# Kernel optimization log

Measured on AMD Instinct MI355X. Metric: run time of the kernel, lower is better.

Reference implementation:

```python
import jax, jax.numpy as jnp
import numpy as np

S, B, C = 7, 2, 20
LAMBDA_COORD = 5.0
LAMBDA_NOOBJ = 0.5
EPS = 1e-6


def _to_abs_xyxy(boxes):
    # boxes: [..., S, S, 4] cell-relative (x,y,w,h) -> normalized image (x1,y1,x2,y2)
    col = jnp.arange(S, dtype=boxes.dtype)            # broadcasts over last grid axis
    row = jnp.arange(S, dtype=boxes.dtype)[:, None]   # broadcasts over second-to-last grid axis
    x, y, w, h = boxes[..., 0], boxes[..., 1], boxes[..., 2], boxes[..., 3]
    cx = (col + x) / S
    cy = (row + y) / S
    return jnp.stack([cx - w / 2, cy - h / 2, cx + w / 2, cy + h / 2], axis=-1)


def _iou(a, b):
    # elementwise IoU of corresponding xyxy boxes (broadcasting allowed)
    x1 = jnp.maximum(a[..., 0], b[..., 0])
    y1 = jnp.maximum(a[..., 1], b[..., 1])
    x2 = jnp.minimum(a[..., 2], b[..., 2])
    y2 = jnp.minimum(a[..., 3], b[..., 3])
    inter = jnp.clip(x2 - x1, 0.0) * jnp.clip(y2 - y1, 0.0)
    area_a = (a[..., 2] - a[..., 0]) * (a[..., 3] - a[..., 1])
    area_b = (b[..., 2] - b[..., 0]) * (b[..., 3] - b[..., 1])
    return inter / (area_a + area_b - inter + EPS)


def setup_inputs() -> dict:
    key = jax.random.key(0)
    kp, kb, kf, kc = jax.random.split(key, 4)
    bs = 16384
    predictions = jax.random.uniform(kp, (bs, S, S, B * 5 + C), dtype=jnp.float32)
    gt_box = jax.random.uniform(kb, (bs, S, S, 4), dtype=jnp.float32)
    obj = (jax.random.uniform(kf, (bs, S, S)) < 0.06).astype(jnp.float32)
    cls = jax.nn.one_hot(jax.random.randint(kc, (bs, S, S), 0, C), C, dtype=jnp.float32)
    targets = jnp.concatenate([gt_box, obj[..., None], cls], axis=-1)
    return {"predictions": predictions, "targets": targets}


def reference(predictions, targets):
    bs = predictions.shape[0]
    pb = predictions[..., : B * 5].reshape(bs, S, S, B, 5)
    boxes = pb[..., :4]                 # [bs,S,S,B,4]
    confs = pb[..., 4]                  # [bs,S,S,B]
    logits = predictions[..., B * 5 :]  # [bs,S,S,C]

    gt_boxes = targets[..., :4]
    objf = (targets[..., 4] > 0).astype(predictions.dtype)  # [bs,S,S]
    gt_cls = targets[..., 5:]

    # IoU per candidate box vs the cell's GT box
    gt_abs = _to_abs_xyxy(gt_boxes)                         # [bs,S,S,4]
    pred_abs = _to_abs_xyxy(jnp.moveaxis(boxes, 3, 1))      # [bs,B,S,S,4]
    ious = jnp.moveaxis(_iou(pred_abs, gt_abs[:, None]), 1, 3)  # [bs,S,S,B]

    best = jnp.argmax(ious, axis=-1)                        # [bs,S,S]
    resp_box = jnp.take_along_axis(boxes, best[..., None, None], axis=3)[..., 0, :]  # [bs,S,S,4]
    resp_conf = jnp.take_along_axis(confs, best[..., None], axis=-1)[..., 0]
    resp_iou = jnp.take_along_axis(ious, best[..., None], axis=-1)[..., 0]

    # Localization loss (masked-sum == torch boolean-mask + sum reduction)
    w = objf[..., None]
    xy_loss = jnp.sum(w * (resp_box[..., :2] - gt_boxes[..., :2]) ** 2)
    wh_loss = jnp.sum(w * (jnp.sqrt(resp_box[..., 2:4] + EPS) - jnp.sqrt(gt_boxes[..., 2:4] + EPS)) ** 2)
    loss_coord = xy_loss + wh_loss

    # Objectness confidence: target is (detached) IoU of responsible box
    loss_conf_obj = jnp.sum(objf * (resp_conf - jax.lax.stop_gradient(resp_iou)) ** 2)

    # No-object confidence: every (cell, box) that is not the responsible box of an object cell
    resp_mask = jax.nn.one_hot(best, B, dtype=predictions.dtype) * objf[..., None]  # [bs,S,S,B]
    loss_conf_noobj = jnp.sum((1.0 - resp_mask) * confs ** 2)

    # Classification: cross-entropy with one-hot GT, summed over object cells
    logp = jax.nn.log_softmax(logits, axis=-1)
    loss_class = -jnp.sum(objf * jnp.sum(gt_cls * logp, axis=-1))

    n = jnp.asarray(bs, predictions.dtype)
    loss_total = (LAMBDA_COORD * loss_coord + loss_conf_obj + LAMBDA_NOOBJ * loss_conf_noobj + loss_class) / n
    # [loss_coord, loss_conf_obj, loss_conf_noobj, loss_class, loss_total]
    return jnp.stack([loss_coord / n, loss_conf_obj / n, loss_conf_noobj / n, loss_class / n, loss_total])
```

## Files before the change

### kernel.cpp

```cpp
#include <hip/hip_runtime.h>
#include <math.h>

namespace {
constexpr int S = 7;
constexpr int B = 2;
constexpr int C = 20;
constexpr int PF = B * 5 + C;
constexpr int TF = 5 + C;
constexpr float EPS = 1e-6f;
constexpr float LAMBDA_COORD = 5.0f;
constexpr float LAMBDA_NOOBJ = 0.5f;
constexpr int BLK = 256;
}

__global__ __launch_bounds__(BLK) void k_main(const float* __restrict__ pred,
                                              const float* __restrict__ tgt,
                                              float* __restrict__ part,
                                              int n_cells) {
    const int tid = threadIdx.x;
    const int cell = blockIdx.x * BLK + tid;

    float v0 = 0.f, v1 = 0.f, v2 = 0.f, v3 = 0.f;
    if (cell < n_cells) {
        const float* p = pred + (size_t)cell * PF;
        const float* t = tgt + (size_t)cell * TF;

        const float2 p45 = *(const float2*)(p + 4);
        const float2 p89 = *(const float2*)(p + 8);
        const float c0 = p45.x, c1 = p89.y;
        const float t4 = t[4];

        v2 = c0 * c0 + c1 * c1;

        if (t4 > 0.f) {
            const int j = cell % S;
            const int i = (cell / S) % S;
            const float invS = 1.0f / (float)S;

            const float2 p01 = *(const float2*)(p + 0);
            const float2 p23 = *(const float2*)(p + 2);
            const float2 p67 = *(const float2*)(p + 6);
            const float gx = t[0], gy = t[1], gw = t[2], gh = t[3];

            const float gcx = ((float)j + gx) * invS;
            const float gcy = ((float)i + gy) * invS;
            const float gx1 = gcx - gw * 0.5f, gy1 = gcy - gh * 0.5f;
            const float gx2 = gcx + gw * 0.5f, gy2 = gcy + gh * 0.5f;
            const float garea = (gx2 - gx1) * (gy2 - gy1);

            const float bx[B]  = {p01.x, p45.y};
            const float by[B]  = {p01.y, p67.x};
            const float bw_[B] = {p23.x, p67.y};
            const float bh[B]  = {p23.y, p89.x};
            const float cf[B]  = {c0, c1};
            float iou[B];
            #pragma unroll
            for (int b = 0; b < B; ++b) {
                const float cx = ((float)j + bx[b]) * invS;
                const float cy = ((float)i + by[b]) * invS;
                const float x1 = cx - bw_[b] * 0.5f, y1 = cy - bh[b] * 0.5f;
                const float x2 = cx + bw_[b] * 0.5f, y2 = cy + bh[b] * 0.5f;
                const float ix1 = fmaxf(x1, gx1), iy1 = fmaxf(y1, gy1);
                const float ix2 = fminf(x2, gx2), iy2 = fminf(y2, gy2);
                const float inter = fmaxf(ix2 - ix1, 0.f) * fmaxf(iy2 - iy1, 0.f);
                const float parea = (x2 - x1) * (y2 - y1);
                iou[b] = inter / (parea + garea - inter + EPS);
            }
            const int best = (iou[1] > iou[0]) ? 1 : 0;
            const float rconf = cf[best], riou = iou[best];

            const float dx = bx[best] - gx, dy = by[best] - gy;
            const float swd = sqrtf(bw_[best] + EPS) - sqrtf(gw + EPS);
            const float shd = sqrtf(bh[best] + EPS) - sqrtf(gh + EPS);
            v0 = dx*dx + dy*dy + swd*swd + shd*shd;
            const float dc = rconf - riou;
            v1 = dc * dc;
            v2 -= rconf * rconf;

            float se = 0.f, dot = 0.f, sg = 0.f;
            #pragma unroll
            for (int c = 0; c < C; c += 2) {
                const float2 lc = *(const float2*)(p + 10 + c);
                const float g0 = t[5 + c], g1 = t[6 + c];
                se  += __expf(lc.x) + __expf(lc.y);
                dot += g0 * lc.x + g1 * lc.y;
                sg  += g0 + g1;
            }
            v3 = __logf(se) * sg - dot;
        }
    }

    float v[4] = {v0, v1, v2, v3};
    #pragma unroll
    for (int off = 32; off >= 1; off >>= 1) {
        v[0] += __shfl_down(v[0], off, 64);
        v[1] += __shfl_down(v[1], off, 64);
        v[2] += __shfl_down(v[2], off, 64);
        v[3] += __shfl_down(v[3], off, 64);
    }
    __shared__ float red[16];
    const int lane = tid & 63;
    const int wave = tid >> 6;
    if (lane == 0) {
        red[wave * 4 + 0] = v[0];
        red[wave * 4 + 1] = v[1];
        red[wave * 4 + 2] = v[2];
        red[wave * 4 + 3] = v[3];
    }
    __syncthreads();
    if (tid < 4)
        part[blockIdx.x * 4 + tid] =
            red[tid] + red[4 + tid] + red[8 + tid] + red[12 + tid];
}

__global__ __launch_bounds__(BLK) void k_fin(const float* __restrict__ part,
                                             float* __restrict__ out,
                                             int nblk, float n) {
    const int tid = threadIdx.x;
    float a0 = 0.f, a1 = 0.f, a2 = 0.f, a3 = 0.f;
    for (int r = tid; r < nblk; r += BLK) {
        const float4 q = *(const float4*)(part + r * 4);
        a0 += q.x; a1 += q.y; a2 += q.z; a3 += q.w;
    }
    float v[4] = {a0, a1, a2, a3};
    #pragma unroll
    for (int off = 32; off >= 1; off >>= 1) {
        v[0] += __shfl_down(v[0], off, 64);
        v[1] += __shfl_down(v[1], off, 64);
        v[2] += __shfl_down(v[2], off, 64);
        v[3] += __shfl_down(v[3], off, 64);
    }
    __shared__ float red[16];
    const int lane = tid & 63;
    const int wave = tid >> 6;
    if (lane == 0) {
        red[wave * 4 + 0] = v[0];
        red[wave * 4 + 1] = v[1];
        red[wave * 4 + 2] = v[2];
        red[wave * 4 + 3] = v[3];
    }
    __syncthreads();
    if (tid == 0) {
        const float coord  = red[0] + red[4] + red[8] + red[12];
        const float cobj   = red[1] + red[5] + red[9] + red[13];
        const float cnoobj = red[2] + red[6] + red[10] + red[14];
        const float ccls   = red[3] + red[7] + red[11] + red[15];
        const float inv = 1.0f / n;
        out[0] = coord * inv;
        out[1] = cobj * inv;
        out[2] = cnoobj * inv;
        out[3] = ccls * inv;
        out[4] = (LAMBDA_COORD * coord + cobj + LAMBDA_NOOBJ * cnoobj + ccls) * inv;
    }
}

extern "C" void kernel_launch(void* const* d_in, const int* in_sizes, int n_in,
                              void* d_out, int out_size, void* d_ws, size_t ws_size,
                              hipStream_t stream) {
    const float* pred = (const float*)d_in[0];
    const float* tgt  = (const float*)d_in[1];
    float* out  = (float*)d_out;
    float* part = (float*)d_ws;

    const int n_cells = in_sizes[0] / PF;
    const float bs = (float)(n_cells / (S * S));
    const int nblk = (n_cells + BLK - 1) / BLK;

    k_main<<<nblk, BLK, 0, stream>>>(pred, tgt, part, n_cells);
    k_fin<<<1, BLK, 0, stream>>>(part, out, nblk, bs);
}
```

Measured before the change: 201.5 us.

## Stream both inputs as coalesced float4 in a grid-stride scan

Replaces the one-thread-per-cell kernel with a fixed-size grid-stride kernel that reads the prediction and target arrays as flat coalesced float4 streams, with several loads in flight per thread. Confidence and objectness values are picked out by their position in each vector. Object cells then re-gather their full prediction and target rows for the IoU and class terms. The goal is fully coalesced bandwidth instead of strided per-cell loads. The cost is extra modulo arithmetic per vector, divergent branches, and a second read of the rows for object cells. Every byte of both arrays is now read, including box and logit fields that no-object cells never needed.

```diff
diff --git a/kernel.cpp b/kernel.cpp
--- a/kernel.cpp
+++ b/kernel.cpp
@@ -3,90 +3,122 @@
 
 namespace {
 constexpr int S = 7;
-constexpr int B = 2;
+constexpr int PF = 30;
+constexpr int TF = 25;
 constexpr int C = 20;
-constexpr int PF = B * 5 + C;
-constexpr int TF = 5 + C;
 constexpr float EPS = 1e-6f;
 constexpr float LAMBDA_COORD = 5.0f;
 constexpr float LAMBDA_NOOBJ = 0.5f;
 constexpr int BLK = 256;
-}
-
-__global__ __launch_bounds__(BLK) void k_main(const float* __restrict__ pred,
+constexpr int ILP = 4;
+constexpr int NBLK = 2048;
+}
+
+__global__ __launch_bounds__(BLK) void k_scan(const float* __restrict__ pred,
                                               const float* __restrict__ tgt,
                                               float* __restrict__ part,
-                                              int n_cells) {
-    const int tid = threadIdx.x;
-    const int cell = blockIdx.x * BLK + tid;
+                                              unsigned np4p, unsigned np4t) {
+    const unsigned tid = threadIdx.x;
+    const unsigned total = np4p + np4t;
+    const unsigned tile = BLK * ILP;
 
     float v0 = 0.f, v1 = 0.f, v2 = 0.f, v3 = 0.f;
-    if (cell < n_cells) {
-        const float* p = pred + (size_t)cell * PF;
-        const float* t = tgt + (size_t)cell * TF;
-
-        const float2 p45 = *(const float2*)(p + 4);
-        const float2 p89 = *(const float2*)(p + 8);
-        const float c0 = p45.x, c1 = p89.y;
-        const float t4 = t[4];
-
-        v2 = c0 * c0 + c1 * c1;
-
-        if (t4 > 0.f) {
-            const int j = cell % S;
-            const int i = (cell / S) % S;
-            const float invS = 1.0f / (float)S;
-
-            const float2 p01 = *(const float2*)(p + 0);
-            const float2 p23 = *(const float2*)(p + 2);
-            const float2 p67 = *(const float2*)(p + 6);
-            const float gx = t[0], gy = t[1], gw = t[2], gh = t[3];
-
-            const float gcx = ((float)j + gx) * invS;
-            const float gcy = ((float)i + gy) * invS;
-            const float gx1 = gcx - gw * 0.5f, gy1 = gcy - gh * 0.5f;
-            const float gx2 = gcx + gw * 0.5f, gy2 = gcy + gh * 0.5f;
-            const float garea = (gx2 - gx1) * (gy2 - gy1);
-
-            const float bx[B]  = {p01.x, p45.y};
-            const float by[B]  = {p01.y, p67.x};
-            const float bw_[B] = {p23.x, p67.y};
-            const float bh[B]  = {p23.y, p89.x};
-            const float cf[B]  = {c0, c1};
-            float iou[B];
-            #pragma unroll
-            for (int b = 0; b < B; ++b) {
-                const float cx = ((float)j + bx[b]) * invS;
-                const float cy = ((float)i + by[b]) * invS;
-                const float x1 = cx - bw_[b] * 0.5f, y1 = cy - bh[b] * 0.5f;
-                const float x2 = cx + bw_[b] * 0.5f, y2 = cy + bh[b] * 0.5f;
-                const float ix1 = fmaxf(x1, gx1), iy1 = fmaxf(y1, gy1);
-                const float ix2 = fminf(x2, gx2), iy2 = fminf(y2, gy2);
-                const float inter = fmaxf(ix2 - ix1, 0.f) * fmaxf(iy2 - iy1, 0.f);
-                const float parea = (x2 - x1) * (y2 - y1);
-                iou[b] = inter / (parea + garea - inter + EPS);
+
+    for (unsigned start = blockIdx.x * tile; start < total; start += gridDim.x * tile) {
+        float4 val[ILP];
+        unsigned qv[ILP];
+        bool okv[ILP], ispv[ILP];
+        #pragma unroll
+        for (int k = 0; k < ILP; ++k) {
+            const unsigned idx = start + (unsigned)k * BLK + tid;
+            const bool ok = idx < total;
+            const bool isp = idx < np4p;
+            const unsigned q = isp ? idx : (idx - np4p);
+            okv[k] = ok; ispv[k] = isp; qv[k] = q;
+            const float4* src = isp ? (const float4*)pred : (const float4*)tgt;
+            val[k] = ok ? src[q] : make_float4(0.f, 0.f, 0.f, 0.f);
+        }
+        #pragma unroll
+        for (int k = 0; k < ILP; ++k) {
+            if (!okv[k]) continue;
+            const float4 v = val[k];
+            const unsigned q = qv[k];
+            if (ispv[k]) {
+                const unsigned r = q % 15u;
+                const float s = (r == 1u) ? v.x
+                              : (r == 2u) ? v.y
+                              : (r == 8u) ? v.z
+                              : (r == 9u) ? v.w : 0.f;
+                v2 += s * s;
+            } else {
+                const unsigned r = q % 25u;
+                const unsigned m = q / 25u;
+                float t4 = 0.f; unsigned cell = 0u;
+                if (r == 1u)       { t4 = v.x; cell = 4u * m; }
+                else if (r == 7u)  { t4 = v.y; cell = 4u * m + 1u; }
+                else if (r == 13u) { t4 = v.z; cell = 4u * m + 2u; }
+                else if (r == 19u) { t4 = v.w; cell = 4u * m + 3u; }
+                if (t4 > 0.f) {
+                    const float* p = pred + (size_t)cell * PF;
+                    const float* t = tgt + (size_t)cell * TF;
+                    const unsigned j = cell % 7u;
+                    const unsigned i = (cell / 7u) % 7u;
+                    const float invS = 1.0f / 7.0f;
+
+                    const float2 p01 = *(const float2*)(p + 0);
+                    const float2 p23 = *(const float2*)(p + 2);
+                    const float2 p45 = *(const float2*)(p + 4);
+                    const float2 p67 = *(const float2*)(p + 6);
+                    const float2 p89 = *(const float2*)(p + 8);
+                    const float gx = t[0], gy = t[1], gw = t[2], gh = t[3];
+
+                    const float gcx = ((float)j + gx) * invS;
+                    const float gcy = ((float)i + gy) * invS;
+                    const float gx1 = gcx - gw * 0.5f, gy1 = gcy - gh * 0.5f;
+                    const float gx2 = gcx + gw * 0.5f, gy2 = gcy + gh * 0.5f;
+                    const float garea = (gx2 - gx1) * (gy2 - gy1);
+
+                    const float bx[2]  = {p01.x, p45.y};
+                    const float by[2]  = {p01.y, p67.x};
+                    const float bw_[2] = {p23.x, p67.y};
+                    const float bh[2]  = {p23.y, p89.x};
+                    const float cf[2]  = {p45.x, p89.y};
+                    float iou[2];
+                    #pragma unroll
+                    for (int b = 0; b < 2; ++b) {
+                        const float cx = ((float)j + bx[b]) * invS;
+                        const float cy = ((float)i + by[b]) * invS;
+                        const float x1 = cx - bw_[b] * 0.5f, y1 = cy - bh[b] * 0.5f;
+                        const float x2 = cx + bw_[b] * 0.5f, y2 = cy + bh[b] * 0.5f;
+                        const float ix1 = fmaxf(x1, gx1), iy1 = fmaxf(y1, gy1);
+                        const float ix2 = fminf(x2, gx2), iy2 = fminf(y2, gy2);
+                        const float inter = fmaxf(ix2 - ix1, 0.f) * fmaxf(iy2 - iy1, 0.f);
+                        const float parea = (x2 - x1) * (y2 - y1);
+                        iou[b] = inter / (parea + garea - inter + EPS);
+                    }
+                    const int best = (iou[1] > iou[0]) ? 1 : 0;
+                    const float rconf = cf[best], riou = iou[best];
+
+                    const float dx = bx[best] - gx, dy = by[best] - gy;
+                    const float swd = sqrtf(bw_[best] + EPS) - sqrtf(gw + EPS);
+                    const float shd = sqrtf(bh[best] + EPS) - sqrtf(gh + EPS);
+                    v0 += dx*dx + dy*dy + swd*swd + shd*shd;
+                    const float dc = rconf - riou;
+                    v1 += dc * dc;
+                    v2 -= rconf * rconf;
+
+                    float se = 0.f, dot = 0.f, sg = 0.f;
+                    #pragma unroll
+                    for (int c = 0; c < C; c += 2) {
+                        const float2 lc = *(const float2*)(p + 10 + c);
+                        const float g0 = t[5 + c], g1 = t[6 + c];
+                        se  += __expf(lc.x) + __expf(lc.y);
+                        dot += g0 * lc.x + g1 * lc.y;
+                        sg  += g0 + g1;
+                    }
+                    v3 += __logf(se) * sg - dot;
+                }
             }
-            const int best = (iou[1] > iou[0]) ? 1 : 0;
-            const float rconf = cf[best], riou = iou[best];
-
-            const float dx = bx[best] - gx, dy = by[best] - gy;
-            const float swd = sqrtf(bw_[best] + EPS) - sqrtf(gw + EPS);
-            const float shd = sqrtf(bh[best] + EPS) - sqrtf(gh + EPS);
-            v0 = dx*dx + dy*dy + swd*swd + shd*shd;
-            const float dc = rconf - riou;
-            v1 = dc * dc;
-            v2 -= rconf * rconf;
-
-            float se = 0.f, dot = 0.f, sg = 0.f;
-            #pragma unroll
-            for (int c = 0; c < C; c += 2) {
-                const float2 lc = *(const float2*)(p + 10 + c);
-                const float g0 = t[5 + c], g1 = t[6 + c];
-                se  += __expf(lc.x) + __expf(lc.y);
-                dot += g0 * lc.x + g1 * lc.y;
-                sg  += g0 + g1;
-            }
-            v3 = __logf(se) * sg - dot;
         }
     }
 
@@ -162,10 +194,11 @@
     float* out  = (float*)d_out;
     float* part = (float*)d_ws;
 
+    const unsigned np4p = (unsigned)(in_sizes[0] / 4);
+    const unsigned np4t = (unsigned)(in_sizes[1] / 4);
     const int n_cells = in_sizes[0] / PF;
     const float bs = (float)(n_cells / (S * S));
-    const int nblk = (n_cells + BLK - 1) / BLK;
-
-    k_main<<<nblk, BLK, 0, stream>>>(pred, tgt, part, n_cells);
-    k_fin<<<1, BLK, 0, stream>>>(part, out, nblk, bs);
-}
+
+    k_scan<<<NBLK, BLK, 0, stream>>>(pred, tgt, part, np4p, np4t);
+    k_fin<<<1, BLK, 0, stream>>>(part, out, NBLK, bs);
+}
```

Result: slower. 218.1 us (+8.2%).

## Split loss into dense no-object scan plus compacted object-cell worklist pass

Applied to the files above, without the earlier changes.

The single per-cell kernel is replaced by a grid-stride scan that reads predictions as coalesced float4 and accumulates confidence squares through per-lane masks, since the 30-float row period fits 15 float4 vectors. The same scan compacts object cells into a worklist with a global atomic counter, and a second kernel processes only those sparse cells to compute IoU, coordinate and class terms. The aim is to remove the strided scalar loads and the divergent work across the dense majority of cells. In exchange it adds extra launches, an atomic per object cell, and a fallback path used when the workspace is too small.

```diff
diff --git a/kernel.cpp b/kernel.cpp
--- a/kernel.cpp
+++ b/kernel.cpp
@@ -3,59 +3,248 @@
 
 namespace {
 constexpr int S = 7;
-constexpr int B = 2;
+constexpr int PF = 30;
+constexpr int TF = 25;
 constexpr int C = 20;
-constexpr int PF = B * 5 + C;
-constexpr int TF = 5 + C;
 constexpr float EPS = 1e-6f;
 constexpr float LAMBDA_COORD = 5.0f;
 constexpr float LAMBDA_NOOBJ = 0.5f;
 constexpr int BLK = 256;
-}
-
-__global__ __launch_bounds__(BLK) void k_main(const float* __restrict__ pred,
+constexpr int ILP = 4;
+constexpr int NBLK = 1875;
+constexpr int NBLK2 = 256;
+
+constexpr int OFF_PART  = 0;
+constexpr int OFF_PART2 = NBLK * 4;
+constexpr int OFF_CNT   = OFF_PART2 + NBLK2 * 4;
+constexpr int OFF_WL    = OFF_CNT + 4;
+}
+
+__global__ void k_zero(int* cnt) {
+    if (threadIdx.x == 0) *cnt = 0;
+}
+
+__global__ __launch_bounds__(BLK) void k_scan(const float4* __restrict__ pred4,
                                               const float* __restrict__ tgt,
                                               float* __restrict__ part,
-                                              int n_cells) {
+                                              int* __restrict__ cnt,
+                                              int* __restrict__ wl,
+                                              unsigned np4p, unsigned n_cells) {
+    const unsigned tid = threadIdx.x;
+    const unsigned stride = (unsigned)NBLK * BLK * ILP;
+    const unsigned base0 = blockIdx.x * (unsigned)(BLK * ILP) + tid;
+
+    float v2 = 0.f;
+
+    float mx[ILP], my[ILP], mz[ILP], mw[ILP];
+    #pragma unroll
+    for (int k = 0; k < ILP; ++k) {
+        const unsigned r = (base0 + (unsigned)k * BLK) % 15u;
+        mx[k] = (r == 1u) ? 1.f : 0.f;
+        my[k] = (r == 2u) ? 1.f : 0.f;
+        mz[k] = (r == 8u) ? 1.f : 0.f;
+        mw[k] = (r == 9u) ? 1.f : 0.f;
+    }
+    for (unsigned s = base0; s < np4p; s += stride) {
+        #pragma unroll
+        for (int k = 0; k < ILP; ++k) {
+            const unsigned idx = s + (unsigned)k * BLK;
+            if (idx < np4p) {
+                const float4 v = pred4[idx];
+                v2 += (mx[k] * v.x) * v.x + (my[k] * v.y) * v.y
+                    + (mz[k] * v.z) * v.z + (mw[k] * v.w) * v.w;
+            }
+        }
+    }
+
+    const unsigned gstride = (unsigned)NBLK * BLK;
+    for (unsigned cell = blockIdx.x * (unsigned)BLK + tid; cell < n_cells; cell += gstride) {
+        const float t4 = tgt[cell * 25u + 4u];
+        if (t4 > 0.f) {
+            const int pos = atomicAdd(cnt, 1);
+            wl[pos] = (int)cell;
+        }
+    }
+
+    #pragma unroll
+    for (int off = 32; off >= 1; off >>= 1) v2 += __shfl_down(v2, off, 64);
+    __shared__ float red[4];
+    if ((tid & 63) == 0) red[tid >> 6] = v2;
+    __syncthreads();
+    if (tid < 4) {
+        const float s2 = red[0] + red[1] + red[2] + red[3];
+        part[blockIdx.x * 4 + tid] = (tid == 2) ? s2 : 0.f;
+    }
+}
+
+__global__ __launch_bounds__(BLK) void k_obj(const float* __restrict__ pred,
+                                             const float* __restrict__ tgt,
+                                             const int* __restrict__ cnt,
+                                             const int* __restrict__ wl,
+                                             float* __restrict__ part2) {
+    const int tid = threadIdx.x;
+    const int n = *cnt;
+    float v0 = 0.f, v1 = 0.f, v2 = 0.f, v3 = 0.f;
+
+    for (int w = blockIdx.x * BLK + tid; w < n; w += NBLK2 * BLK) {
+        const unsigned cell = (unsigned)wl[w];
+        const float* p = pred + (size_t)cell * PF;
+        const float* t = tgt + (size_t)cell * TF;
+        const unsigned j = cell % 7u;
+        const unsigned i = (cell / 7u) % 7u;
+        const float invS = 1.0f / 7.0f;
+
+        const float2 p01 = *(const float2*)(p + 0);
+        const float2 p23 = *(const float2*)(p + 2);
+        const float2 p45 = *(const float2*)(p + 4);
+        const float2 p67 = *(const float2*)(p + 6);
+        const float2 p89 = *(const float2*)(p + 8);
+        const float gx = t[0], gy = t[1], gw = t[2], gh = t[3];
+
+        const float gcx = ((float)j + gx) * invS;
+        const float gcy = ((float)i + gy) * invS;
+        const float gx1 = gcx - gw * 0.5f, gy1 = gcy - gh * 0.5f;
+        const float gx2 = gcx + gw * 0.5f, gy2 = gcy + gh * 0.5f;
+        const float garea = (gx2 - gx1) * (gy2 - gy1);
+
+        const float bx[2]  = {p01.x, p45.y};
+        const float by[2]  = {p01.y, p67.x};
+        const float bw_[2] = {p23.x, p67.y};
+        const float bh[2]  = {p23.y, p89.x};
+        const float cf[2]  = {p45.x, p89.y};
+        float iou[2];
+        #pragma unroll
+        for (int b = 0; b < 2; ++b) {
+            const float cx = ((float)j + bx[b]) * invS;
+            const float cy = ((float)i + by[b]) * invS;
+            const float x1 = cx - bw_[b] * 0.5f, y1 = cy - bh[b] * 0.5f;
+            const float x2 = cx + bw_[b] * 0.5f, y2 = cy + bh[b] * 0.5f;
+            const float ix1 = fmaxf(x1, gx1), iy1 = fmaxf(y1, gy1);
+            const float ix2 = fminf(x2, gx2), iy2 = fminf(y2, gy2);
+            const float inter = fmaxf(ix2 - ix1, 0.f) * fmaxf(iy2 - iy1, 0.f);
+            const float parea = (x2 - x1) * (y2 - y1);
+            iou[b] = inter / (parea + garea - inter + EPS);
+        }
+        const int best = (iou[1] > iou[0]) ? 1 : 0;
+        const float rconf = cf[best], riou = iou[best];
+
+        const float dx = bx[best] - gx, dy = by[best] - gy;
+        const float swd = sqrtf(bw_[best] + EPS) - sqrtf(gw + EPS);
+        const float shd = sqrtf(bh[best] + EPS) - sqrtf(gh + EPS);
+        v0 += dx * dx + dy * dy + swd * swd + shd * shd;
+        const float dc = rconf - riou;
+        v1 += dc * dc;
+        v2 -= rconf * rconf;
+
+        float se = 0.f, dot = 0.f, sg = 0.f;
+        #pragma unroll
+        for (int c = 0; c < C; c += 2) {
+            const float2 lc = *(const float2*)(p + 10 + c);
+            const float g0 = t[5 + c], g1 = t[6 + c];
+            se  += __expf(lc.x) + __expf(lc.y);
+            dot += g0 * lc.x + g1 * lc.y;
+            sg  += g0 + g1;
+        }
+        v3 += __logf(se) * sg - dot;
+    }
+
+    float v[4] = {v0, v1, v2, v3};
+    #pragma unroll
+    for (int off = 32; off >= 1; off >>= 1) {
+        v[0] += __shfl_down(v[0], off, 64);
+        v[1] += __shfl_down(v[1], off, 64);
+        v[2] += __shfl_down(v[2], off, 64);
+        v[3] += __shfl_down(v[3], off, 64);
+    }
+    __shared__ float red[16];
+    if ((tid & 63) == 0) {
+        const int wv = tid >> 6;
+        red[wv * 4 + 0] = v[0];
+        red[wv * 4 + 1] = v[1];
+        red[wv * 4 + 2] = v[2];
+        red[wv * 4 + 3] = v[3];
+    }
+    __syncthreads();
+    if (tid < 4)
+        part2[blockIdx.x * 4 + tid] =
+            red[tid] + red[4 + tid] + red[8 + tid] + red[12 + tid];
+}
+
+__global__ __launch_bounds__(BLK) void k_fin(const float* __restrict__ part,
+                                             float* __restrict__ out,
+                                             int nslots, float n) {
+    const int tid = threadIdx.x;
+    float a0 = 0.f, a1 = 0.f, a2 = 0.f, a3 = 0.f;
+    for (int r = tid; r < nslots; r += BLK) {
+        const float4 q = *(const float4*)(part + r * 4);
+        a0 += q.x; a1 += q.y; a2 += q.z; a3 += q.w;
+    }
+    float v[4] = {a0, a1, a2, a3};
+    #pragma unroll
+    for (int off = 32; off >= 1; off >>= 1) {
+        v[0] += __shfl_down(v[0], off, 64);
+        v[1] += __shfl_down(v[1], off, 64);
+        v[2] += __shfl_down(v[2], off, 64);
+        v[3] += __shfl_down(v[3], off, 64);
+    }
+    __shared__ float red[16];
+    if ((tid & 63) == 0) {
+        const int wv = tid >> 6;
+        red[wv * 4 + 0] = v[0];
+        red[wv * 4 + 1] = v[1];
+        red[wv * 4 + 2] = v[2];
+        red[wv * 4 + 3] = v[3];
+    }
+    __syncthreads();
+    if (tid == 0) {
+        const float coord  = red[0] + red[4] + red[8] + red[12];
+        const float cobj   = red[1] + red[5] + red[9] + red[13];
+        const float cnoobj = red[2] + red[6] + red[10] + red[14];
+        const float ccls   = red[3] + red[7] + red[11] + red[15];
+        const float inv = 1.0f / n;
+        out[0] = coord * inv;
+        out[1] = cobj * inv;
+        out[2] = cnoobj * inv;
+        out[3] = ccls * inv;
+        out[4] = (LAMBDA_COORD * coord + cobj + LAMBDA_NOOBJ * cnoobj + ccls) * inv;
+    }
+}
+
+__global__ __launch_bounds__(BLK) void k_main_fb(const float* __restrict__ pred,
+                                                 const float* __restrict__ tgt,
+                                                 float* __restrict__ part,
+                                                 int n_cells) {
     const int tid = threadIdx.x;
     const int cell = blockIdx.x * BLK + tid;
-
     float v0 = 0.f, v1 = 0.f, v2 = 0.f, v3 = 0.f;
     if (cell < n_cells) {
         const float* p = pred + (size_t)cell * PF;
         const float* t = tgt + (size_t)cell * TF;
-
         const float2 p45 = *(const float2*)(p + 4);
         const float2 p89 = *(const float2*)(p + 8);
         const float c0 = p45.x, c1 = p89.y;
-        const float t4 = t[4];
-
         v2 = c0 * c0 + c1 * c1;
-
-        if (t4 > 0.f) {
+        if (t[4] > 0.f) {
             const int j = cell % S;
             const int i = (cell / S) % S;
             const float invS = 1.0f / (float)S;
-
             const float2 p01 = *(const float2*)(p + 0);
             const float2 p23 = *(const float2*)(p + 2);
             const float2 p67 = *(const float2*)(p + 6);
             const float gx = t[0], gy = t[1], gw = t[2], gh = t[3];
-
             const float gcx = ((float)j + gx) * invS;
             const float gcy = ((float)i + gy) * invS;
             const float gx1 = gcx - gw * 0.5f, gy1 = gcy - gh * 0.5f;
             const float gx2 = gcx + gw * 0.5f, gy2 = gcy + gh * 0.5f;
             const float garea = (gx2 - gx1) * (gy2 - gy1);
-
-            const float bx[B]  = {p01.x, p45.y};
-            const float by[B]  = {p01.y, p67.x};
-            const float bw_[B] = {p23.x, p67.y};
-            const float bh[B]  = {p23.y, p89.x};
-            const float cf[B]  = {c0, c1};
-            float iou[B];
+            const float bx[2]  = {p01.x, p45.y};
+            const float by[2]  = {p01.y, p67.x};
+            const float bw_[2] = {p23.x, p67.y};
+            const float bh[2]  = {p23.y, p89.x};
+            const float cf[2]  = {c0, c1};
+            float iou[2];
             #pragma unroll
-            for (int b = 0; b < B; ++b) {
+            for (int b = 0; b < 2; ++b) {
                 const float cx = ((float)j + bx[b]) * invS;
                 const float cy = ((float)i + by[b]) * invS;
                 const float x1 = cx - bw_[b] * 0.5f, y1 = cy - bh[b] * 0.5f;
@@ -68,7 +257,6 @@
             }
             const int best = (iou[1] > iou[0]) ? 1 : 0;
             const float rconf = cf[best], riou = iou[best];
-
             const float dx = bx[best] - gx, dy = by[best] - gy;
             const float swd = sqrtf(bw_[best] + EPS) - sqrtf(gw + EPS);
             const float shd = sqrtf(bh[best] + EPS) - sqrtf(gh + EPS);
@@ -76,7 +264,6 @@
             const float dc = rconf - riou;
             v1 = dc * dc;
             v2 -= rconf * rconf;
-
             float se = 0.f, dot = 0.f, sg = 0.f;
             #pragma unroll
             for (int c = 0; c < C; c += 2) {
@@ -89,7 +276,6 @@
             v3 = __logf(se) * sg - dot;
         }
     }
-
     float v[4] = {v0, v1, v2, v3};
     #pragma unroll
     for (int off = 32; off >= 1; off >>= 1) {
@@ -99,59 +285,17 @@
         v[3] += __shfl_down(v[3], off, 64);
     }
     __shared__ float red[16];
-    const int lane = tid & 63;
-    const int wave = tid >> 6;
-    if (lane == 0) {
-        red[wave * 4 + 0] = v[0];
-        red[wave * 4 + 1] = v[1];
-        red[wave * 4 + 2] = v[2];
-        red[wave * 4 + 3] = v[3];
+    if ((tid & 63) == 0) {
+        const int wv = tid >> 6;
+        red[wv * 4 + 0] = v[0];
+        red[wv * 4 + 1] = v[1];
+        red[wv * 4 + 2] = v[2];
+        red[wv * 4 + 3] = v[3];
     }
     __syncthreads();
     if (tid < 4)
         part[blockIdx.x * 4 + tid] =
             red[tid] + red[4 + tid] + red[8 + tid] + red[12 + tid];
-}
-
-__global__ __launch_bounds__(BLK) void k_fin(const float* __restrict__ part,
-                                             float* __restrict__ out,
-                                             int nblk, float n) {
-    const int tid = threadIdx.x;
-    float a0 = 0.f, a1 = 0.f, a2 = 0.f, a3 = 0.f;
-    for (int r = tid; r < nblk; r += BLK) {
-        const float4 q = *(const float4*)(part + r * 4);
-        a0 += q.x; a1 += q.y; a2 += q.z; a3 += q.w;
-    }
-    float v[4] = {a0, a1, a2, a3};
-    #pragma unroll
-    for (int off = 32; off >= 1; off >>= 1) {
-        v[0] += __shfl_down(v[0], off, 64);
-        v[1] += __shfl_down(v[1], off, 64);
-        v[2] += __shfl_down(v[2], off, 64);
-        v[3] += __shfl_down(v[3], off, 64);
-    }
-    __shared__ float red[16];
-    const int lane = tid & 63;
-    const int wave = tid >> 6;
-    if (lane == 0) {
-        red[wave * 4 + 0] = v[0];
-        red[wave * 4 + 1] = v[1];
-        red[wave * 4 + 2] = v[2];
-        red[wave * 4 + 3] = v[3];
-    }
-    __syncthreads();
-    if (tid == 0) {
-        const float coord  = red[0] + red[4] + red[8] + red[12];
-        const float cobj   = red[1] + red[5] + red[9] + red[13];
-        const float cnoobj = red[2] + red[6] + red[10] + red[14];
-        const float ccls   = red[3] + red[7] + red[11] + red[15];
-        const float inv = 1.0f / n;
-        out[0] = coord * inv;
-        out[1] = cobj * inv;
-        out[2] = cnoobj * inv;
-        out[3] = ccls * inv;
-        out[4] = (LAMBDA_COORD * coord + cobj + LAMBDA_NOOBJ * cnoobj + ccls) * inv;
-    }
 }
 
 extern "C" void kernel_launch(void* const* d_in, const int* in_sizes, int n_in,
@@ -159,13 +303,27 @@
                               hipStream_t stream) {
     const float* pred = (const float*)d_in[0];
     const float* tgt  = (const float*)d_in[1];
-    float* out  = (float*)d_out;
-    float* part = (float*)d_ws;
+    float* out = (float*)d_out;
+    float* ws  = (float*)d_ws;
 
     const int n_cells = in_sizes[0] / PF;
+    const unsigned np4p = (unsigned)(in_sizes[0] / 4);
     const float bs = (float)(n_cells / (S * S));
-    const int nblk = (n_cells + BLK - 1) / BLK;
-
-    k_main<<<nblk, BLK, 0, stream>>>(pred, tgt, part, n_cells);
-    k_fin<<<1, BLK, 0, stream>>>(part, out, nblk, bs);
-}
+
+    const size_t need = (size_t)(OFF_WL + n_cells) * sizeof(float);
+    if (ws_size >= need) {
+        float* part  = ws + OFF_PART;
+        float* part2 = ws + OFF_PART2;
+        int*   cnt   = (int*)(ws + OFF_CNT);
+        int*   wl    = (int*)(ws + OFF_WL);
+        k_zero<<<1, 64, 0, stream>>>(cnt);
+        k_scan<<<NBLK, BLK, 0, stream>>>((const float4*)pred, tgt, part, cnt, wl,
+                                         np4p, (unsigned)n_cells);
+        k_obj<<<NBLK2, BLK, 0, stream>>>(pred, tgt, cnt, wl, part2);
+        k_fin<<<1, BLK, 0, stream>>>(part, out, NBLK + NBLK2, bs);
+    } else {
+        const int nblk = (n_cells + BLK - 1) / BLK;
+        k_main_fb<<<nblk, BLK, 0, stream>>>(pred, tgt, ws, n_cells);
+        k_fin<<<1, BLK, 0, stream>>>(ws, out, nblk, bs);
+    }
+}
```

Result: slower. 320.3 us (+58.9%).
